# Optimization experiments

Hardware: AMD Instinct MI355X
Metric: run time of the kernel (lower is better)

The kernel has to match this reference:

```python
import jax, jax.numpy as jnp
import numpy as np

B, S, D = 8, 2048, 256
H = 4
DH = D // H  # 64


def setup_inputs() -> dict:
    key = jax.random.key(0)
    ks = jax.random.split(key, 6)
    x = jax.random.normal(ks[0], (B, S, D), dtype=jnp.float32)
    # Linear weights stored as (d_in, d_out) so y = x @ W (+ b)
    scale = 1.0 / np.sqrt(D)
    w_q = jax.random.normal(ks[1], (D, D), dtype=jnp.float32) * scale
    w_k = jax.random.normal(ks[2], (D, D), dtype=jnp.float32) * scale
    w_v = jax.random.normal(ks[3], (D, D), dtype=jnp.float32) * scale
    w_o = jax.random.normal(ks[4], (D, D), dtype=jnp.float32) * scale
    b_o = jax.random.normal(ks[5], (D,), dtype=jnp.float32) * 0.01
    return {"x": x, "w_q": w_q, "w_k": w_k, "w_v": w_v, "w_o": w_o, "b_o": b_o}


def reference(x, w_q, w_k, w_v, w_o, b_o):
    b, s, _ = x.shape
    # project and split heads: [b, h, s, dh]
    q = (x @ w_q).reshape(b, s, H, DH).transpose(0, 2, 1, 3)
    k = (x @ w_k).reshape(b, s, H, DH).transpose(0, 2, 1, 3)
    v = (x @ w_v).reshape(b, s, H, DH).transpose(0, 2, 1, 3)
    # full attention matrix [b, h, s, s] (matches original non-fused math)
    scores = jnp.einsum('bhqd,bhkd->bhqk', q, k) / jnp.sqrt(jnp.float32(DH))
    attn = jax.nn.softmax(scores, axis=-1)  # dropout is identity in eval
    ctx = jnp.einsum('bhqk,bhkd->bhqd', attn, v)
    ctx = ctx.transpose(0, 2, 1, 3).reshape(b, s, H * DH)
    return ctx @ w_o + b_o
```

## Files before the change

### kernel.cpp

```cpp
#include <hip/hip_runtime.h>
#include <hip/hip_fp16.h>
#include <math.h>

typedef _Float16 f16;
typedef _Float16 f16x8 __attribute__((ext_vector_type(8)));
typedef float f32x4 __attribute__((ext_vector_type(4)));
typedef float f32x16 __attribute__((ext_vector_type(16)));
typedef unsigned int u32;
typedef unsigned int u32x4 __attribute__((ext_vector_type(4)));

#define BB 8
#define SS 2048
#define DD 256
#define HH 4
#define DHH 64

#define LOG2E 1.44269504088896340736f
#define MOFF2 (4.0f * LOG2E)
#define QSCALE (0.125f * LOG2E)

static __device__ __forceinline__ u32 pkrtz(float a, float b) {
  auto t = __builtin_amdgcn_cvt_pkrtz(a, b);
  return __builtin_bit_cast(u32, t);
}

__global__ __launch_bounds__(256) void prep_kernel(
    const float* __restrict__ wq, const float* __restrict__ wk,
    const float* __restrict__ wv, const float* __restrict__ wo,
    f16* __restrict__ wqkvT, f16* __restrict__ woT) {
  __shared__ f16 lds[64][72];
  int dout0 = blockIdx.x * 64;
  int k0 = blockIdx.y * 64;
  const float* src;
  f16* dst;
  int col0, drow;
  if (dout0 < 256)      { src = wq; dst = wqkvT; col0 = dout0;       drow = dout0; }
  else if (dout0 < 512) { src = wk; dst = wqkvT; col0 = dout0 - 256; drow = dout0; }
  else if (dout0 < 768) { src = wv; dst = wqkvT; col0 = dout0 - 512; drow = dout0; }
  else                  { src = wo; dst = woT;   col0 = dout0 - 768; drow = dout0 - 768; }

  int dl = threadIdx.x & 63, kl = threadIdx.x >> 6;
#pragma unroll
  for (int i = 0; i < 16; i++) {
    int kloc = i * 4 + kl;
    lds[kloc][dl] = (f16)src[(size_t)(k0 + kloc) * 256 + col0 + dl];
  }
  __syncthreads();
  int row_l = threadIdx.x >> 2, kq = threadIdx.x & 3;
  f16x8 v0, v1;
#pragma unroll
  for (int j = 0; j < 8; j++) v0[j] = lds[kq * 16 + j][row_l];
#pragma unroll
  for (int j = 0; j < 8; j++) v1[j] = lds[kq * 16 + 8 + j][row_l];
  f16* p = dst + (size_t)(drow + row_l) * 256 + k0 + kq * 16;
  *(f16x8*)p = v0;
  *(f16x8*)(p + 8) = v1;
}

__global__ __launch_bounds__(256) void qkv_gemm(
    const float* __restrict__ x, const f16* __restrict__ wT,
    f16* __restrict__ Q, f16* __restrict__ K, f16* __restrict__ VT) {
  __shared__ __attribute__((aligned(16))) f16 bstage[8][4][64][8];
  __shared__ __attribute__((aligned(16))) f16 lds_t[64][72];
  int m0 = blockIdx.x * 64;
  int which = blockIdx.y;
  int nbase = which * 256;
  int wave = threadIdx.x >> 6, lane = threadIdx.x & 63;
  int lm = lane & 15, quad = lane >> 4;
  float qsc = (which == 0) ? QSCALE : 1.0f;

  const float* arow = x + (size_t)(m0 + wave * 16 + lm) * 256 + quad * 8;
  f16x8 a[8];
#pragma unroll
  for (int kk = 0; kk < 8; kk++) {
    f32x4 a0 = *(const f32x4*)(arow + kk * 32);
    f32x4 a1 = *(const f32x4*)(arow + kk * 32 + 4);
#pragma unroll
    for (int j = 0; j < 4; j++) { a[kk][j] = (f16)a0[j]; a[kk][j + 4] = (f16)a1[j]; }
  }

  f16x8 breg[8];
  auto bload = [&](int n0) {
#pragma unroll
    for (int kk = 0; kk < 8; kk++)
      breg[kk] = *(const f16x8*)(wT + (size_t)(n0 + wave * 16 + lm) * 256 + kk * 32 + quad * 8);
  };
  bload(nbase);

  int bb = m0 >> 11, s0 = m0 & 2047;
  for (int i = 0; i < 4; i++) {
    int n0 = nbase + i * 64;
#pragma unroll
    for (int kk = 0; kk < 8; kk++)
      *(f16x8*)&bstage[kk][wave][lane][0] = breg[kk];
    __syncthreads();
    if (i + 1 < 4) bload(nbase + (i + 1) * 64);

    f32x4 acc[4] = {};
#pragma unroll
    for (int kk = 0; kk < 8; kk++)
#pragma unroll
      for (int nt = 0; nt < 4; nt++) {
        f16x8 b = *(const f16x8*)&bstage[kk][nt][lane][0];
        acc[nt] = __builtin_amdgcn_mfma_f32_16x16x32_f16(a[kk], b, acc[nt], 0, 0, 0);
      }

    if (which < 2) {
      f16* dst = (which == 0) ? Q : K;
      int nb = n0 & 255;
#pragma unroll
      for (int nt = 0; nt < 4; nt++) {
        int dout = nb + nt * 16 + lm;
        int h = dout >> 6, dh = dout & 63;
#pragma unroll
        for (int r = 0; r < 4; r++) {
          int s = s0 + wave * 16 + quad * 4 + r;
          dst[(((size_t)(bb * HH + h) * SS + s) << 6) + dh] = (f16)(acc[nt][r] * qsc);
        }
      }
    } else {
      int h = i;
#pragma unroll
      for (int nt = 0; nt < 4; nt++)
#pragma unroll
        for (int r = 0; r < 4; r++)
          lds_t[nt * 16 + lm][wave * 16 + quad * 4 + r] = (f16)acc[nt][r];
      __syncthreads();
      int rr = threadIdx.x >> 2, cc = threadIdx.x & 3;
      f16* vrow = VT + ((size_t)(bb * HH + h) * DHH + rr) * SS + s0;
      f16x8 v0 = *(const f16x8*)&lds_t[rr][cc * 16];
      f16x8 v1 = *(const f16x8*)&lds_t[rr][cc * 16 + 8];
      *(f16x8*)(vrow + cc * 16) = v0;
      *(f16x8*)(vrow + cc * 16 + 8) = v1;
    }
    __syncthreads();
  }
}

__global__ __launch_bounds__(512, 2) void attn_kernel(
    const f16* __restrict__ Q, const f16* __restrict__ K,
    const f16* __restrict__ VT, f16* __restrict__ ctx) {
  __shared__ __attribute__((aligned(16))) f16 kv[2][2][2][8][64][8];

  int qb = blockIdx.x, hd = blockIdx.y, b = blockIdx.z;
  int w = threadIdx.x >> 6, lane = threadIdx.x & 63;
  int half = w >> 2, wl = w & 3;
  int l31 = lane & 31, hi = lane >> 5, hi8 = hi * 8;
  const f16* Qbh = Q + (size_t)(b * HH + hd) * SS * DHH;
  const f16* Kbh = K + (size_t)(b * HH + hd) * SS * DHH;
  const f16* Vbh = VT + (size_t)(b * HH + hd) * DHH * SS;
  int q0 = qb * 128 + wl * 32;
  int kh0 = half * 1024;

  f16x8 tk0, tk1, tv0, tv1;
  auto stage_load = [&](int key0) {
    tk0 = *(const f16x8*)(Kbh + (size_t)(key0 + l31) * DHH + wl * 16 + hi8);
    tk1 = *(const f16x8*)(Kbh + (size_t)(key0 + 32 + l31) * DHH + wl * 16 + hi8);
    tv0 = *(const f16x8*)(Vbh + (size_t)l31 * SS + key0 + wl * 16 + hi8);
    tv1 = *(const f16x8*)(Vbh + (size_t)(32 + l31) * SS + key0 + wl * 16 + hi8);
  };
  auto stage_write = [&](int buf) {
    *(f16x8*)&kv[half][buf][0][wl][lane][0] = tk0;
    *(f16x8*)&kv[half][buf][0][4 + wl][lane][0] = tk1;
    *(f16x8*)&kv[half][buf][1][wl][lane][0] = tv0;
    *(f16x8*)&kv[half][buf][1][4 + wl][lane][0] = tv1;
  };

  f16x8 aq[4];
  {
    const f16* qrow = Qbh + (size_t)(q0 + l31) * DHH + hi8;
#pragma unroll
    for (int kp = 0; kp < 4; kp++) aq[kp] = *(const f16x8*)(qrow + kp * 16);
  }
  f16x8 vones;
#pragma unroll
  for (int j = 0; j < 8; j++) vones[j] = (f16)1.0f;
  f32x16 minit;
#pragma unroll
  for (int r = 0; r < 16; r++) minit[r] = -MOFF2;

  f32x16 accO0, accO1, accL;
#pragma unroll
  for (int r = 0; r < 16; r++) { accO0[r] = 0.f; accO1[r] = 0.f; accL[r] = 0.f; }

  stage_load(kh0);
  stage_write(0);
  stage_load(kh0 + 64);

  const int NT = 1024 / 64;
  for (int t = 0; t < NT; t++) {
    int cur = t & 1;
    __syncthreads();

    if (t + 1 < NT) {
      stage_write(cur ^ 1);
      if (t + 2 < NT) stage_load(kh0 + (t + 2) * 64);
    }

    f32x16 accST[2];
#pragma unroll
    for (int kp = 0; kp < 4; kp++)
#pragma unroll
      for (int nt = 0; nt < 2; nt++) {
        f16x8 kf = *(const f16x8*)&kv[half][cur][0][nt * 4 + kp][lane][0];
        accST[nt] = __builtin_amdgcn_mfma_f32_32x32x16_f16(
            kf, aq[kp], kp == 0 ? minit : accST[nt], 0, 0, 0);
      }

    f16x8 pa[4];
#pragma unroll
    for (int nt = 0; nt < 2; nt++) {
      u32 u[4][2];
#pragma unroll
      for (int bq = 0; bq < 4; bq++) {
        float p0 = __builtin_amdgcn_exp2f(accST[nt][4 * bq + 0]);
        float p1 = __builtin_amdgcn_exp2f(accST[nt][4 * bq + 1]);
        float p2 = __builtin_amdgcn_exp2f(accST[nt][4 * bq + 2]);
        float p3 = __builtin_amdgcn_exp2f(accST[nt][4 * bq + 3]);
        u[bq][0] = pkrtz(p0, p1);
        u[bq][1] = pkrtz(p2, p3);
      }
#pragma unroll
      for (int sl = 0; sl < 2; sl++) {
        auto r0 = __builtin_amdgcn_permlane32_swap(u[2 * sl][0], u[2 * sl + 1][0],
                                                   false, false);
        auto r1 = __builtin_amdgcn_permlane32_swap(u[2 * sl][1], u[2 * sl + 1][1],
                                                   false, false);
        u32x4 wv = {(u32)r0[0], (u32)r1[0], (u32)r0[1], (u32)r1[1]};
        pa[nt * 2 + sl] = __builtin_bit_cast(f16x8, wv);
      }
    }

#pragma unroll
    for (int ks = 0; ks < 4; ks++) {
      accL = __builtin_amdgcn_mfma_f32_32x32x16_f16(pa[ks], vones, accL, 0, 0, 0);
      f16x8 v0 = *(const f16x8*)&kv[half][cur][1][ks][lane][0];
      accO0 = __builtin_amdgcn_mfma_f32_32x32x16_f16(pa[ks], v0, accO0, 0, 0, 0);
      f16x8 v1 = *(const f16x8*)&kv[half][cur][1][4 + ks][lane][0];
      accO1 = __builtin_amdgcn_mfma_f32_32x32x16_f16(pa[ks], v1, accO1, 0, 0, 0);
    }
  }

  __syncthreads();
  float* scratch = (float*)kv;
  int sbase = (wl * 64 + lane) * 49;
  if (half == 1) {
#pragma unroll
    for (int r = 0; r < 16; r++) {
      scratch[sbase + r]      = accO0[r];
      scratch[sbase + 16 + r] = accO1[r];
      scratch[sbase + 32 + r] = accL[r];
    }
  }
  __syncthreads();
  if (half == 0) {
#pragma unroll
    for (int r = 0; r < 16; r++) {
      float o0 = accO0[r] + scratch[sbase + r];
      float o1 = accO1[r] + scratch[sbase + 16 + r];
      float rinv = __builtin_amdgcn_rcpf(accL[r] + scratch[sbase + 32 + r]);
      int s = q0 + (r & 3) + 8 * (r >> 2) + 4 * hi;
      f16* dst = ctx + (size_t)(b * SS + s) * DD + hd * DHH + l31;
      dst[0]  = (f16)(o0 * rinv);
      dst[32] = (f16)(o1 * rinv);
    }
  }
}

__global__ __launch_bounds__(256) void out_gemm(
    const f16* __restrict__ ctxh, const f16* __restrict__ woT,
    const float* __restrict__ bo, float* __restrict__ out) {
  __shared__ __attribute__((aligned(16))) f16 bstage[8][4][64][8];
  int m0 = blockIdx.x * 64;
  int nbase = blockIdx.y * 128;
  int wave = threadIdx.x >> 6, lane = threadIdx.x & 63;
  int lm = lane & 15, quad = lane >> 4;
  const f16* arow = ctxh + (size_t)(m0 + wave * 16 + lm) * 256 + quad * 8;
  f16x8 a[8];
#pragma unroll
  for (int kk = 0; kk < 8; kk++) a[kk] = *(const f16x8*)(arow + kk * 32);

  f16x8 breg[8];
  auto bload = [&](int n0) {
#pragma unroll
    for (int kk = 0; kk < 8; kk++)
      breg[kk] = *(const f16x8*)(woT + (size_t)(n0 + wave * 16 + lm) * 256 + kk * 32 + quad * 8);
  };
  bload(nbase);

  for (int i = 0; i < 2; i++) {
    int n0 = nbase + i * 64;
#pragma unroll
    for (int kk = 0; kk < 8; kk++)
      *(f16x8*)&bstage[kk][wave][lane][0] = breg[kk];
    __syncthreads();
    if (i + 1 < 2) bload(nbase + 64);

    f32x4 acc[4] = {};
#pragma unroll
    for (int kk = 0; kk < 8; kk++)
#pragma unroll
      for (int nt = 0; nt < 4; nt++) {
        f16x8 bfr = *(const f16x8*)&bstage[kk][nt][lane][0];
        acc[nt] = __builtin_amdgcn_mfma_f32_16x16x32_f16(a[kk], bfr, acc[nt], 0, 0, 0);
      }
#pragma unroll
    for (int nt = 0; nt < 4; nt++) {
      int dout = n0 + nt * 16 + lm;
      float bias = bo[dout];
#pragma unroll
      for (int r = 0; r < 4; r++) {
        int t = m0 + wave * 16 + quad * 4 + r;
        out[(size_t)t * 256 + dout] = acc[nt][r] + bias;
      }
    }
    __syncthreads();
  }
}

extern "C" void kernel_launch(void* const* d_in, const int* in_sizes, int n_in,
                              void* d_out, int out_size, void* d_ws, size_t ws_size,
                              hipStream_t stream) {
  const float* x  = (const float*)d_in[0];
  const float* wq = (const float*)d_in[1];
  const float* wk = (const float*)d_in[2];
  const float* wv = (const float*)d_in[3];
  const float* wo = (const float*)d_in[4];
  const float* bo = (const float*)d_in[5];
  float* out = (float*)d_out;

  char* ws = (char*)d_ws;
  const size_t SZ = 8388608;
  f16* Qb    = (f16*)(ws);
  f16* Kb    = (f16*)(ws + SZ);
  f16* VTb   = (f16*)(ws + 2 * SZ);
  f16* ctxh  = (f16*)(ws + 3 * SZ);
  f16* wqkvT = (f16*)(ws + 4 * SZ);
  f16* woT   = (f16*)(ws + 4 * SZ + 393216);

  hipLaunchKernelGGL(prep_kernel, dim3(16, 4), dim3(256), 0, stream,
                     wq, wk, wv, wo, wqkvT, woT);
  hipLaunchKernelGGL(qkv_gemm, dim3(256, 3), dim3(256), 0, stream,
                     x, wqkvT, Qb, Kb, VTb);
  hipLaunchKernelGGL(attn_kernel, dim3(16, 4, 8), dim3(512), 0, stream,
                     Qb, Kb, VTb, ctxh);
  hipLaunchKernelGGL(out_gemm, dim3(256, 2), dim3(256), 0, stream,
                     ctxh, woT, bo, out);
}
```

Before: 155.9 us.

## Compute full N per block in QKV and output GEMMs with LDS-staged A tiles

Each QKV GEMM block now covers all 768 output columns, and each output GEMM block all 256, so the input row tile of x or ctx is read from global memory and converted once instead of three or two times. A rows are loaded with coalesced row-wise reads into an LDS staging buffer in MFMA fragment order. Q and K stores now go through an LDS transpose, which turns the scattered per-element f16 writes into 16-byte vector stores. In exchange, the grids shrink to 256 blocks, each running a longer serial loop with extra syncs and more LDS, which lowers parallelism across the GPU.

```diff
diff --git a/kernel.cpp b/kernel.cpp
--- a/kernel.cpp
+++ b/kernel.cpp
@@ -60,24 +60,33 @@
 __global__ __launch_bounds__(256) void qkv_gemm(
     const float* __restrict__ x, const f16* __restrict__ wT,
     f16* __restrict__ Q, f16* __restrict__ K, f16* __restrict__ VT) {
+  __shared__ __attribute__((aligned(16))) f16 astage[8][4][64][8];
   __shared__ __attribute__((aligned(16))) f16 bstage[8][4][64][8];
   __shared__ __attribute__((aligned(16))) f16 lds_t[64][72];
   int m0 = blockIdx.x * 64;
-  int which = blockIdx.y;
-  int nbase = which * 256;
   int wave = threadIdx.x >> 6, lane = threadIdx.x & 63;
   int lm = lane & 15, quad = lane >> 4;
-  float qsc = (which == 0) ? QSCALE : 1.0f;
-
-  const float* arow = x + (size_t)(m0 + wave * 16 + lm) * 256 + quad * 8;
+  int bb = m0 >> 11, s0 = m0 & 2047;
+
+  {
+    int row = threadIdx.x >> 2;
+    int c0 = (threadIdx.x & 3) * 64;
+    const float* xr = x + (size_t)(m0 + row) * 256 + c0;
+#pragma unroll
+    for (int i = 0; i < 8; i++) {
+      f32x4 lo = *(const f32x4*)(xr + i * 8);
+      f32x4 hi = *(const f32x4*)(xr + i * 8 + 4);
+      f16x8 v;
+#pragma unroll
+      for (int j = 0; j < 4; j++) { v[j] = (f16)lo[j]; v[j + 4] = (f16)hi[j]; }
+      int col = c0 + i * 8;
+      *(f16x8*)&astage[col >> 5][row >> 4][((col >> 3) & 3) * 16 + (row & 15)][0] = v;
+    }
+  }
+  __syncthreads();
   f16x8 a[8];
 #pragma unroll
-  for (int kk = 0; kk < 8; kk++) {
-    f32x4 a0 = *(const f32x4*)(arow + kk * 32);
-    f32x4 a1 = *(const f32x4*)(arow + kk * 32 + 4);
-#pragma unroll
-    for (int j = 0; j < 4; j++) { a[kk][j] = (f16)a0[j]; a[kk][j + 4] = (f16)a1[j]; }
-  }
+  for (int kk = 0; kk < 8; kk++) a[kk] = *(const f16x8*)&astage[kk][wave][lane][0];
 
   f16x8 breg[8];
   auto bload = [&](int n0) {
@@ -85,16 +94,14 @@
     for (int kk = 0; kk < 8; kk++)
       breg[kk] = *(const f16x8*)(wT + (size_t)(n0 + wave * 16 + lm) * 256 + kk * 32 + quad * 8);
   };
-  bload(nbase);
-
-  int bb = m0 >> 11, s0 = m0 & 2047;
-  for (int i = 0; i < 4; i++) {
-    int n0 = nbase + i * 64;
+  bload(0);
+
+  for (int i = 0; i < 12; i++) {
 #pragma unroll
     for (int kk = 0; kk < 8; kk++)
       *(f16x8*)&bstage[kk][wave][lane][0] = breg[kk];
     __syncthreads();
-    if (i + 1 < 4) bload(nbase + (i + 1) * 64);
+    if (i + 1 < 12) bload((i + 1) * 64);
 
     f32x4 acc[4] = {};
 #pragma unroll
@@ -105,21 +112,21 @@
         acc[nt] = __builtin_amdgcn_mfma_f32_16x16x32_f16(a[kk], b, acc[nt], 0, 0, 0);
       }
 
-    if (which < 2) {
-      f16* dst = (which == 0) ? Q : K;
-      int nb = n0 & 255;
-#pragma unroll
-      for (int nt = 0; nt < 4; nt++) {
-        int dout = nb + nt * 16 + lm;
-        int h = dout >> 6, dh = dout & 63;
-#pragma unroll
-        for (int r = 0; r < 4; r++) {
-          int s = s0 + wave * 16 + quad * 4 + r;
-          dst[(((size_t)(bb * HH + h) * SS + s) << 6) + dh] = (f16)(acc[nt][r] * qsc);
-        }
-      }
+    int h = i & 3;
+    if (i < 8) {
+      float qsc = (i < 4) ? QSCALE : 1.0f;
+#pragma unroll
+      for (int nt = 0; nt < 4; nt++)
+#pragma unroll
+        for (int r = 0; r < 4; r++)
+          lds_t[wave * 16 + quad * 4 + r][nt * 16 + lm] = (f16)(acc[nt][r] * qsc);
+      __syncthreads();
+      int rr = threadIdx.x >> 2, cc = threadIdx.x & 3;
+      f16* dst = ((i < 4) ? Q : K) +
+                 (((size_t)(bb * HH + h) * SS + s0 + rr) << 6) + cc * 16;
+      *(f16x8*)dst = *(const f16x8*)&lds_t[rr][cc * 16];
+      *(f16x8*)(dst + 8) = *(const f16x8*)&lds_t[rr][cc * 16 + 8];
     } else {
-      int h = i;
 #pragma unroll
       for (int nt = 0; nt < 4; nt++)
 #pragma unroll
@@ -128,10 +135,8 @@
       __syncthreads();
       int rr = threadIdx.x >> 2, cc = threadIdx.x & 3;
       f16* vrow = VT + ((size_t)(bb * HH + h) * DHH + rr) * SS + s0;
-      f16x8 v0 = *(const f16x8*)&lds_t[rr][cc * 16];
-      f16x8 v1 = *(const f16x8*)&lds_t[rr][cc * 16 + 8];
-      *(f16x8*)(vrow + cc * 16) = v0;
-      *(f16x8*)(vrow + cc * 16 + 8) = v1;
+      *(f16x8*)(vrow + cc * 16) = *(const f16x8*)&lds_t[rr][cc * 16];
+      *(f16x8*)(vrow + cc * 16 + 8) = *(const f16x8*)&lds_t[rr][cc * 16 + 8];
     }
     __syncthreads();
   }
@@ -270,15 +275,27 @@
 __global__ __launch_bounds__(256) void out_gemm(
     const f16* __restrict__ ctxh, const f16* __restrict__ woT,
     const float* __restrict__ bo, float* __restrict__ out) {
+  __shared__ __attribute__((aligned(16))) f16 astage[8][4][64][8];
   __shared__ __attribute__((aligned(16))) f16 bstage[8][4][64][8];
   int m0 = blockIdx.x * 64;
-  int nbase = blockIdx.y * 128;
   int wave = threadIdx.x >> 6, lane = threadIdx.x & 63;
   int lm = lane & 15, quad = lane >> 4;
-  const f16* arow = ctxh + (size_t)(m0 + wave * 16 + lm) * 256 + quad * 8;
+
+  {
+    int row = threadIdx.x >> 2;
+    int c0 = (threadIdx.x & 3) * 64;
+    const f16* cr = ctxh + (size_t)(m0 + row) * 256 + c0;
+#pragma unroll
+    for (int i = 0; i < 8; i++) {
+      f16x8 v = *(const f16x8*)(cr + i * 8);
+      int col = c0 + i * 8;
+      *(f16x8*)&astage[col >> 5][row >> 4][((col >> 3) & 3) * 16 + (row & 15)][0] = v;
+    }
+  }
+  __syncthreads();
   f16x8 a[8];
 #pragma unroll
-  for (int kk = 0; kk < 8; kk++) a[kk] = *(const f16x8*)(arow + kk * 32);
+  for (int kk = 0; kk < 8; kk++) a[kk] = *(const f16x8*)&astage[kk][wave][lane][0];
 
   f16x8 breg[8];
   auto bload = [&](int n0) {
@@ -286,15 +303,15 @@
     for (int kk = 0; kk < 8; kk++)
       breg[kk] = *(const f16x8*)(woT + (size_t)(n0 + wave * 16 + lm) * 256 + kk * 32 + quad * 8);
   };
-  bload(nbase);
-
-  for (int i = 0; i < 2; i++) {
-    int n0 = nbase + i * 64;
+  bload(0);
+
+  for (int i = 0; i < 4; i++) {
+    int n0 = i * 64;
 #pragma unroll
     for (int kk = 0; kk < 8; kk++)
       *(f16x8*)&bstage[kk][wave][lane][0] = breg[kk];
     __syncthreads();
-    if (i + 1 < 2) bload(nbase + 64);
+    if (i + 1 < 4) bload((i + 1) * 64);
 
     f32x4 acc[4] = {};
 #pragma unroll
@@ -340,10 +357,10 @@
 
   hipLaunchKernelGGL(prep_kernel, dim3(16, 4), dim3(256), 0, stream,
                      wq, wk, wv, wo, wqkvT, woT);
-  hipLaunchKernelGGL(qkv_gemm, dim3(256, 3), dim3(256), 0, stream,
+  hipLaunchKernelGGL(qkv_gemm, dim3(256), dim3(256), 0, stream,
                      x, wqkvT, Qb, Kb, VTb);
   hipLaunchKernelGGL(attn_kernel, dim3(16, 4, 8), dim3(512), 0, stream,
                      Qb, Kb, VTb, ctxh);
-  hipLaunchKernelGGL(out_gemm, dim3(256, 2), dim3(256), 0, stream,
+  hipLaunchKernelGGL(out_gemm, dim3(256), dim3(256), 0, stream,
                      ctxh, woT, bo, out);
 }
```

Result: no change. 156.3 us (+0.2%).
